# Optimization experiments

Hardware: AMD Instinct MI355X
Metric: run time of the kernel (lower is better)

## Reference

```python
import jax, jax.numpy as jnp
import numpy as np

# Standard asymmetric NF4 value table (bitsandbytes / flute nf_utils, bits=4, symmetric=False)
NF4_VALUES = np.array([
    -1.0, -0.6961928009986877, -0.5250730514526367, -0.39491748809814453,
    -0.28444138169288635, -0.18477343022823334, -0.09105003625154495, 0.0,
    0.07958029955625534, 0.16093020141124725, 0.2461123913526535,
    0.33791524171829224, 0.44070982933044434, 0.5626170039176941,
    0.7229568362236023, 1.0], dtype=np.float32)
# Pivots are midpoints between consecutive values -> nearest-value bucketing via searchsorted
NF4_PIVOTS = (NF4_VALUES[:-1] + NF4_VALUES[1:]) / 2.0

GROUP_SIZE = 64
IN_FEATURES = 4096
OUT_FEATURES = 4096
BATCH, SEQ = 4, 2048


def setup_inputs() -> dict:
    key = jax.random.key(0)
    k1, k2 = jax.random.split(key)
    inp = jax.random.normal(k1, (BATCH, SEQ, IN_FEATURES), dtype=jnp.float32)
    weight = jax.random.normal(k2, (OUT_FEATURES, IN_FEATURES), dtype=jnp.float32) * 0.02
    # scales initialized exactly as in __init__: per-group absmax of the weight
    scales = jnp.max(jnp.abs(weight.reshape(-1, GROUP_SIZE)), axis=1, keepdims=True)  # [out*in/64, 1]
    return {
        "inp": inp,
        "weight": weight,
        "scales": scales,
        "values": jnp.asarray(NF4_VALUES),
        "pivots": jnp.asarray(NF4_PIVOTS),
    }


def _manual_nf4(weight, scales, values, pivots, group_size):
    # groupwise absmax-normalize, nearest-value lookup via pivot search, dequantize
    w = weight.reshape(-1, group_size)                 # [n_groups, group_size]
    scaled = jnp.clip(w / scales, -1.0, 1.0)
    idx = jnp.searchsorted(pivots, scaled)             # nearest NF4 code
    qweight = values[idx] * scales                     # dequantized bf16-style weight
    return qweight.reshape(weight.shape)


def reference(inp, weight, scales, values, pivots):
    qweight = _manual_nf4(weight, scales, values, pivots, GROUP_SIZE)  # [out, in]
    # F.linear(inp, qweight), bias=None
    return jnp.einsum('bsi,oi->bso', inp, qweight)
```

## Files before the change

kernel.cpp:

```cpp
#include <hip/hip_runtime.h>
#include <hip/hip_bf16.h>
#include <stdint.h>

#define M_DIM 8192
#define N_DIM 4096
#define K_DIM 4096
#define BM 128
#define BN 128
#define BK 64

#define CVT_BLOCKS 8192
#define DQ_BLOCKS  8192

typedef float f32x4 __attribute__((ext_vector_type(4)));
typedef float f32x16 __attribute__((ext_vector_type(16)));
typedef __bf16 bf16x8 __attribute__((ext_vector_type(8)));
typedef short s16x8 __attribute__((ext_vector_type(8)));

template <typename AB>
__device__ __forceinline__ auto mfma_32x32x16(AB a, AB b, f32x16 c, int)
    -> decltype(__builtin_amdgcn_mfma_f32_32x32x16_bf16(a, b, c, 0, 0, 0)) {
  return __builtin_amdgcn_mfma_f32_32x32x16_bf16(a, b, c, 0, 0, 0);
}
template <typename AB>
__device__ __forceinline__ f32x16 mfma_32x32x16(AB a, AB b, f32x16 c, long) {
  return __builtin_amdgcn_mfma_f32_32x32x16_bf16(
      __builtin_bit_cast(s16x8, a), __builtin_bit_cast(s16x8, b), c, 0, 0, 0);
}

__device__ __forceinline__ uint16_t f2b(float f) {
  union { float f; uint32_t u; } v; v.f = f;
  uint32_t u = v.u;
  u += 0x7FFFu + ((u >> 16) & 1u);
  return (uint16_t)(u >> 16);
}

__device__ __forceinline__ void load16_lds(const uint16_t* g, uint16_t* l) {
  __builtin_amdgcn_global_load_lds(
      (__attribute__((address_space(1))) void*)(void*)g,
      (__attribute__((address_space(3))) void*)l, 16, 0, 0);
}

__global__ __launch_bounds__(256) void prep(const float* __restrict__ inp,
                                            uint16_t* __restrict__ A_bf16,
                                            const float* __restrict__ w,
                                            const float* __restrict__ scales,
                                            const float* __restrict__ values,
                                            const float* __restrict__ pivots,
                                            uint16_t* __restrict__ B_bf16) {
  if (blockIdx.x < CVT_BLOCKS) {
    size_t t = (size_t)blockIdx.x * blockDim.x + threadIdx.x;
    const float4* p = (const float4*)inp + t * 4;
    uint4* q = (uint4*)A_bf16 + t * 2;
#pragma unroll
    for (int h = 0; h < 2; ++h) {
      float4 a = p[2 * h], b = p[2 * h + 1];
      uint4 o;
      o.x = (uint32_t)f2b(a.x) | ((uint32_t)f2b(a.y) << 16);
      o.y = (uint32_t)f2b(a.z) | ((uint32_t)f2b(a.w) << 16);
      o.z = (uint32_t)f2b(b.x) | ((uint32_t)f2b(b.y) << 16);
      o.w = (uint32_t)f2b(b.z) | ((uint32_t)f2b(b.w) << 16);
      q[h] = o;
    }
  } else {
    __shared__ float sv[16];
    if (threadIdx.x < 16) sv[threadIdx.x] = values[threadIdx.x];
    float pv[15];
#pragma unroll
    for (int j = 0; j < 15; ++j) pv[j] = pivots[j];
    __syncthreads();
    size_t t = (size_t)(blockIdx.x - CVT_BLOCKS) * blockDim.x + threadIdx.x;
    size_t base = t * 8;
    float scale = scales[base >> 6];
    float psc[15];
#pragma unroll
    for (int j = 0; j < 15; ++j) psc[j] = pv[j] * scale;
    const float4* p = (const float4*)(w + base);
    float4 a = p[0], b = p[1];
    float e[8] = {a.x, a.y, a.z, a.w, b.x, b.y, b.z, b.w};
    uint32_t words[4];
#pragma unroll
    for (int i = 0; i < 4; ++i) {
      uint32_t hw[2];
#pragma unroll
      for (int h = 0; h < 2; ++h) {
        float x = e[2 * i + h];
        int idx = 0;
#pragma unroll
        for (int j = 0; j < 15; ++j) idx += (psc[j] < x) ? 1 : 0;
        hw[h] = f2b(sv[idx] * scale);
      }
      words[i] = hw[0] | (hw[1] << 16);
    }
    uint4 o = {words[0], words[1], words[2], words[3]};
    ((uint4*)B_bf16)[t] = o;
  }
}

__global__ __launch_bounds__(256) void gemm_bt(const uint16_t* __restrict__ A,
                                               const uint16_t* __restrict__ B,
                                               float* __restrict__ C) {
  __shared__ uint16_t As[BM * BK];
  __shared__ uint16_t Bs[BN * BK];
  const int tid = threadIdx.x;
  const int wave = tid >> 6;
  const int lane = tid & 63;
  const int bm = blockIdx.y;
  const int bn = blockIdx.x;

  const int lr = lane >> 3;
  const int lc = (lane & 7) ^ lr;
  const uint16_t* ag[4];
  const uint16_t* bg[4];
  uint16_t* al[4];
  uint16_t* bl[4];
#pragma unroll
  for (int i = 0; i < 4; ++i) {
    int row = wave * 32 + i * 8 + lr;
    ag[i] = A + (size_t)(bm * BM + row) * K_DIM + lc * 8;
    bg[i] = B + (size_t)(bn * BN + row) * K_DIM + lc * 8;
    al[i] = &As[(wave * 32 + i * 8) * BK];
    bl[i] = &Bs[(wave * 32 + i * 8) * BK];
  }

  const int wm = (wave >> 1) * 64;
  const int wn = (wave & 1) * 64;
  const int r31 = lane & 31;
  const int kh = lane >> 5;

  f32x16 acc[2][2] = {};

  for (int k0 = 0; k0 < K_DIM; k0 += BK) {
#pragma unroll
    for (int i = 0; i < 4; ++i) load16_lds(ag[i] + k0, al[i]);
#pragma unroll
    for (int i = 0; i < 4; ++i) load16_lds(bg[i] + k0, bl[i]);
    __syncthreads();
#pragma unroll
    for (int ks = 0; ks < 4; ++ks) {
      const int csl = ((ks * 2 + kh) ^ (r31 & 7)) * 8;
      bf16x8 af[2], bf[2];
#pragma unroll
      for (int i = 0; i < 2; ++i) af[i] = *(const bf16x8*)&As[(wm + i * 32 + r31) * BK + csl];
#pragma unroll
      for (int j = 0; j < 2; ++j) bf[j] = *(const bf16x8*)&Bs[(wn + j * 32 + r31) * BK + csl];
#pragma unroll
      for (int i = 0; i < 2; ++i)
#pragma unroll
        for (int j = 0; j < 2; ++j)
          acc[i][j] = mfma_32x32x16(af[i], bf[j], acc[i][j], 0);
    }
    __syncthreads();
  }

  const int crow0 = bm * BM + wm;
  const int ccol0 = bn * BN + wn + r31;
#pragma unroll
  for (int i = 0; i < 2; ++i)
#pragma unroll
    for (int j = 0; j < 2; ++j)
#pragma unroll
      for (int reg = 0; reg < 16; ++reg) {
        int row = i * 32 + (reg & 3) + 8 * (reg >> 2) + 4 * kh;
        C[(size_t)(crow0 + row) * N_DIM + ccol0 + j * 32] = acc[i][j][reg];
      }
}

extern "C" void kernel_launch(void* const* d_in, const int* in_sizes, int n_in,
                              void* d_out, int out_size, void* d_ws, size_t ws_size,
                              hipStream_t stream) {
  const float* inp    = (const float*)d_in[0];
  const float* weight = (const float*)d_in[1];
  const float* scales = (const float*)d_in[2];
  const float* values = (const float*)d_in[3];
  const float* pivots = (const float*)d_in[4];
  float* out = (float*)d_out;

  uint16_t* A_bf16 = (uint16_t*)d_ws;
  uint16_t* B_bf16 = A_bf16 + (size_t)M_DIM * K_DIM;

  prep<<<CVT_BLOCKS + DQ_BLOCKS, 256, 0, stream>>>(inp, A_bf16, weight, scales, values,
                                                   pivots, B_bf16);
  dim3 grid(N_DIM / BN, M_DIM / BM);
  gemm_bt<<<grid, 256, 0, stream>>>(A_bf16, B_bf16, out);
}
```

Baseline: 549.6 us.

## Rewrite GEMM with 256x256 tiles, 8 waves, double-buffered LDS ping-pong pipeline

Replaces the simple 128x128 single-buffer GEMM with a 256x256 tile per 512-thread block. It double-buffers 128KB of LDS, issues global-to-LDS loads for the next K tile interleaved with the MFMA phases, and uses explicit barriers, vmcnt waits and setprio to overlap memory with compute. It also remaps block IDs in an XCD-aware order for L2 locality and changes the LDS swizzle. The cost is higher register and LDS usage, which limits occupancy, and more fragile hand-scheduled synchronisation.

Result: no change. 546.3 us (-0.6%).

```diff
diff --git a/kernel.cpp b/kernel.cpp
--- a/kernel.cpp
+++ b/kernel.cpp
@@ -5,14 +5,14 @@
 #define M_DIM 8192
 #define N_DIM 4096
 #define K_DIM 4096
-#define BM 128
-#define BN 128
+#define BM 256
+#define BN 256
 #define BK 64
+#define NT (K_DIM / BK)
 
 #define CVT_BLOCKS 8192
 #define DQ_BLOCKS  8192
 
-typedef float f32x4 __attribute__((ext_vector_type(4)));
 typedef float f32x16 __attribute__((ext_vector_type(16)));
 typedef __bf16 bf16x8 __attribute__((ext_vector_type(8)));
 typedef short s16x8 __attribute__((ext_vector_type(8)));
@@ -33,12 +33,6 @@
   uint32_t u = v.u;
   u += 0x7FFFu + ((u >> 16) & 1u);
   return (uint16_t)(u >> 16);
-}
-
-__device__ __forceinline__ void load16_lds(const uint16_t* g, uint16_t* l) {
-  __builtin_amdgcn_global_load_lds(
-      (__attribute__((address_space(1))) void*)(void*)g,
-      (__attribute__((address_space(3))) void*)l, 16, 0, 0);
 }
 
 __global__ __launch_bounds__(256) void prep(const float* __restrict__ inp,
@@ -97,71 +91,168 @@
   }
 }
 
-__global__ __launch_bounds__(256) void gemm_bt(const uint16_t* __restrict__ A,
-                                               const uint16_t* __restrict__ B,
-                                               float* __restrict__ C) {
-  __shared__ uint16_t As[BM * BK];
-  __shared__ uint16_t Bs[BN * BK];
+
+#define GLL(SRC, LOFF)                                                        \
+  __builtin_amdgcn_global_load_lds(                                           \
+      (__attribute__((address_space(1))) void*)(void*)(SRC),                  \
+      (__attribute__((address_space(3))) void*)(smem + (LOFF)), 16, 0, 0)
+
+#define STAGE_A(NB, KH, KEL)                                                  \
+  do {                                                                        \
+    GLL(Ab + gs0 + (KEL) + (KH) * 32, (NB) * 32768u + (KH) * 16384u + l0);    \
+    GLL(Ab + gs1 + (KEL) + (KH) * 32, (NB) * 32768u + (KH) * 16384u + l1);    \
+  } while (0)
+#define STAGE_B(NB, KH, KEL)                                                  \
+  do {                                                                        \
+    GLL(Bb + gs0 + (KEL) + (KH) * 32,                                         \
+        65536u + (NB) * 32768u + (KH) * 16384u + l0);                         \
+    GLL(Bb + gs1 + (KEL) + (KH) * 32,                                         \
+        65536u + (NB) * 32768u + (KH) * 16384u + l1);                         \
+  } while (0)
+
+#define MIDBAR()                                                              \
+  do {                                                                        \
+    asm volatile("" ::: "memory");                                            \
+    __builtin_amdgcn_s_barrier();                                             \
+    __builtin_amdgcn_sched_barrier(0);                                        \
+  } while (0)
+#define VM4BAR()                                                              \
+  do {                                                                        \
+    asm volatile("s_waitcnt vmcnt(4)" ::: "memory");                          \
+    __builtin_amdgcn_s_barrier();                                             \
+    __builtin_amdgcn_sched_barrier(0);                                        \
+  } while (0)
+
+#define PHASE0(CUR, NB, KH, KEL)                                              \
+  do {                                                                        \
+    const uint32_t _ab = (CUR) * 32768u + (KH) * 16384u + aoff;               \
+    const uint32_t _bb = 65536u + (CUR) * 32768u + (KH) * 16384u + boff;      \
+    bf16x8 a00 = *(const bf16x8*)(smem + _ab + cb0);                          \
+    bf16x8 a10 = *(const bf16x8*)(smem + _ab + 2048u + cb0);                  \
+    bf16x8 a01 = *(const bf16x8*)(smem + _ab + cb1);                          \
+    bf16x8 a11 = *(const bf16x8*)(smem + _ab + 2048u + cb1);                  \
+    b00 = *(const bf16x8*)(smem + _bb + cb0);                                 \
+    b10 = *(const bf16x8*)(smem + _bb + 2048u + cb0);                         \
+    b01 = *(const bf16x8*)(smem + _bb + cb1);                                 \
+    b11 = *(const bf16x8*)(smem + _bb + 2048u + cb1);                         \
+    STAGE_A(NB, KH, KEL);                                                     \
+    MIDBAR();                                                                 \
+    __builtin_amdgcn_s_setprio(1);                                            \
+    acc[0][0] = mfma_32x32x16(a00, b00, acc[0][0], 0);                        \
+    acc[0][1] = mfma_32x32x16(a00, b10, acc[0][1], 0);                        \
+    acc[1][0] = mfma_32x32x16(a10, b00, acc[1][0], 0);                        \
+    acc[1][1] = mfma_32x32x16(a10, b10, acc[1][1], 0);                        \
+    acc[0][0] = mfma_32x32x16(a01, b01, acc[0][0], 0);                        \
+    acc[0][1] = mfma_32x32x16(a01, b11, acc[0][1], 0);                        \
+    acc[1][0] = mfma_32x32x16(a11, b01, acc[1][0], 0);                        \
+    acc[1][1] = mfma_32x32x16(a11, b11, acc[1][1], 0);                        \
+    __builtin_amdgcn_sched_barrier(0);                                        \
+    __builtin_amdgcn_s_setprio(0);                                            \
+    MIDBAR();                                                                 \
+  } while (0)
+
+#define PHASE1(CUR, NB, KH, KEL)                                              \
+  do {                                                                        \
+    const uint32_t _ab = (CUR) * 32768u + (KH) * 16384u + aoff + 4096u;       \
+    bf16x8 a00 = *(const bf16x8*)(smem + _ab + cb0);                          \
+    bf16x8 a10 = *(const bf16x8*)(smem + _ab + 2048u + cb0);                  \
+    bf16x8 a01 = *(const bf16x8*)(smem + _ab + cb1);                          \
+    bf16x8 a11 = *(const bf16x8*)(smem + _ab + 2048u + cb1);                  \
+    STAGE_B(NB, KH, KEL);                                                     \
+    MIDBAR();                                                                 \
+    __builtin_amdgcn_s_setprio(1);                                            \
+    acc[2][0] = mfma_32x32x16(a00, b00, acc[2][0], 0);                        \
+    acc[2][1] = mfma_32x32x16(a00, b10, acc[2][1], 0);                        \
+    acc[3][0] = mfma_32x32x16(a10, b00, acc[3][0], 0);                        \
+    acc[3][1] = mfma_32x32x16(a10, b10, acc[3][1], 0);                        \
+    acc[2][0] = mfma_32x32x16(a01, b01, acc[2][0], 0);                        \
+    acc[2][1] = mfma_32x32x16(a01, b11, acc[2][1], 0);                        \
+    acc[3][0] = mfma_32x32x16(a11, b01, acc[3][0], 0);                        \
+    acc[3][1] = mfma_32x32x16(a11, b11, acc[3][1], 0);                        \
+    __builtin_amdgcn_sched_barrier(0);                                        \
+    __builtin_amdgcn_s_setprio(0);                                            \
+    VM4BAR();                                                                 \
+  } while (0)
+
+__global__ __launch_bounds__(512, 2) void gemm_bt(const uint16_t* __restrict__ A,
+                                                  const uint16_t* __restrict__ B,
+                                                  float* __restrict__ C) {
+  __shared__ char smem[131072];
   const int tid = threadIdx.x;
   const int wave = tid >> 6;
   const int lane = tid & 63;
-  const int bm = blockIdx.y;
-  const int bn = blockIdx.x;
-
-  const int lr = lane >> 3;
-  const int lc = (lane & 7) ^ lr;
-  const uint16_t* ag[4];
-  const uint16_t* bg[4];
-  uint16_t* al[4];
-  uint16_t* bl[4];
-#pragma unroll
-  for (int i = 0; i < 4; ++i) {
-    int row = wave * 32 + i * 8 + lr;
-    ag[i] = A + (size_t)(bm * BM + row) * K_DIM + lc * 8;
-    bg[i] = B + (size_t)(bn * BN + row) * K_DIM + lc * 8;
-    al[i] = &As[(wave * 32 + i * 8) * BK];
-    bl[i] = &Bs[(wave * 32 + i * 8) * BK];
+
+  const int bid = blockIdx.x;
+  const int wg = (bid & 7) * 64 + (bid >> 3);
+  const int bm = wg >> 4;
+  const int bn = wg & 15;
+
+  const int wm = wave >> 2;
+  const int wn = wave & 3;
+  const int r31 = lane & 31;
+  const int hi = lane >> 5;
+
+  const int swz = (r31 >> 1) & 3;
+  const uint32_t cb0 = (uint32_t)(((hi ^ swz) * 16));
+  const uint32_t cb1 = (uint32_t)((((2 + hi) ^ swz) * 16));
+  const uint32_t aoff = (uint32_t)(wm * 8192 + r31 * 64);
+  const uint32_t boff = (uint32_t)(wn * 4096 + r31 * 64);
+
+  const int s0 = wave * 128 + lane;
+  const int r0 = s0 >> 2;
+  const uint32_t gs0 =
+      (uint32_t)r0 * K_DIM + (uint32_t)((((s0 & 3) ^ ((r0 >> 1) & 3)) * 8));
+  const int s1 = s0 + 64;
+  const int r1 = s1 >> 2;
+  const uint32_t gs1 =
+      (uint32_t)r1 * K_DIM + (uint32_t)((((s1 & 3) ^ ((r1 >> 1) & 3)) * 8));
+  const uint32_t l0 = (uint32_t)(wave * 2048);
+  const uint32_t l1 = l0 + 1024u;
+
+  const uint16_t* Ab = A + (size_t)bm * BM * K_DIM;
+  const uint16_t* Bb = B + (size_t)bn * BN * K_DIM;
+
+  f32x16 acc[4][2] = {};
+
+  STAGE_A(0u, 0u, 0u);
+  STAGE_B(0u, 0u, 0u);
+  STAGE_A(0u, 1u, 0u);
+  STAGE_B(0u, 1u, 0u);
+  asm volatile("s_waitcnt vmcnt(4)" ::: "memory");
+  __builtin_amdgcn_s_barrier();
+  __builtin_amdgcn_sched_barrier(0);
+
+  for (int kt2 = 0; kt2 < NT; kt2 += 2) {
+    const uint32_t kel0 = (uint32_t)(kt2 + 1) * BK;
+    const uint32_t kel1 =
+        (uint32_t)((kt2 + 2 < NT) ? (kt2 + 2) : (NT - 1)) * BK;
+    {
+      bf16x8 b00, b10, b01, b11;
+      PHASE0(0u, 1u, 0u, kel0);
+      PHASE1(0u, 1u, 0u, kel0);
+      PHASE0(0u, 1u, 1u, kel0);
+      PHASE1(0u, 1u, 1u, kel0);
+    }
+    {
+      bf16x8 b00, b10, b01, b11;
+      PHASE0(1u, 0u, 0u, kel1);
+      PHASE1(1u, 0u, 0u, kel1);
+      PHASE0(1u, 0u, 1u, kel1);
+      PHASE1(1u, 0u, 1u, kel1);
+    }
   }
 
-  const int wm = (wave >> 1) * 64;
-  const int wn = (wave & 1) * 64;
-  const int r31 = lane & 31;
-  const int kh = lane >> 5;
-
-  f32x16 acc[2][2] = {};
-
-  for (int k0 = 0; k0 < K_DIM; k0 += BK) {
-#pragma unroll
-    for (int i = 0; i < 4; ++i) load16_lds(ag[i] + k0, al[i]);
-#pragma unroll
-    for (int i = 0; i < 4; ++i) load16_lds(bg[i] + k0, bl[i]);
-    __syncthreads();
-#pragma unroll
-    for (int ks = 0; ks < 4; ++ks) {
-      const int csl = ((ks * 2 + kh) ^ (r31 & 7)) * 8;
-      bf16x8 af[2], bf[2];
-#pragma unroll
-      for (int i = 0; i < 2; ++i) af[i] = *(const bf16x8*)&As[(wm + i * 32 + r31) * BK + csl];
-#pragma unroll
-      for (int j = 0; j < 2; ++j) bf[j] = *(const bf16x8*)&Bs[(wn + j * 32 + r31) * BK + csl];
-#pragma unroll
-      for (int i = 0; i < 2; ++i)
-#pragma unroll
-        for (int j = 0; j < 2; ++j)
-          acc[i][j] = mfma_32x32x16(af[i], bf[j], acc[i][j], 0);
-    }
-    __syncthreads();
-  }
-
-  const int crow0 = bm * BM + wm;
-  const int ccol0 = bn * BN + wn + r31;
-#pragma unroll
-  for (int i = 0; i < 2; ++i)
+  asm volatile("s_waitcnt vmcnt(0)" ::: "memory");
+
+  const int crow0 = bm * BM + wm * 128;
+  const int ccol0 = bn * BN + wn * 64 + r31;
+#pragma unroll
+  for (int i = 0; i < 4; ++i)
 #pragma unroll
     for (int j = 0; j < 2; ++j)
 #pragma unroll
       for (int reg = 0; reg < 16; ++reg) {
-        int row = i * 32 + (reg & 3) + 8 * (reg >> 2) + 4 * kh;
+        int row = i * 32 + (reg & 3) + 8 * (reg >> 2) + 4 * hi;
         C[(size_t)(crow0 + row) * N_DIM + ccol0 + j * 32] = acc[i][j][reg];
       }
 }
@@ -181,6 +272,5 @@
 
   prep<<<CVT_BLOCKS + DQ_BLOCKS, 256, 0, stream>>>(inp, A_bf16, weight, scales, values,
                                                    pivots, B_bf16);
-  dim3 grid(N_DIM / BN, M_DIM / BM);
-  gemm_bt<<<grid, 256, 0, stream>>>(A_bf16, B_bf16, out);
-}
+  gemm_bt<<<dim3(512), 512, 0, stream>>>(A_bf16, B_bf16, out);
+}
```
